# Optimization experiments

Measured on AMD Instinct MI355X. Metric: run time of the kernel, lower is better.

The kernel has to match this reference:

```python
import jax, jax.numpy as jnp
import numpy as np

H, D = 8, 32            # num_heads, per-head out_dim (same for C1/C2/C3/state)
ALPHA = 0.2             # leaky-relu negative slope
N_C, N_S = 10000, 1024  # nodes per C type, state nodes
E_CC, E_CS = 120000, 10000
IN_C, IN_S = 128, 64


def setup_inputs() -> dict:
    key = jax.random.key(0)
    ks = jax.random.split(key, 20)
    xn = lambda k, sh, s=1.0: jax.random.normal(k, sh, dtype=jnp.float32) * s
    inp = {}
    inp["feat_C1"] = xn(ks[0], (N_C, IN_C))
    inp["feat_C2"] = xn(ks[1], (N_C, IN_C))
    inp["feat_C3"] = xn(ks[2], (N_C, IN_C))
    inp["feat_state"] = xn(ks[3], (N_S, IN_S))
    # linear weights (xavier-ish scale) and zero biases
    inp["W_node"] = xn(ks[4], (3, IN_C, H * D), 0.06)
    inp["b_node"] = jnp.zeros((3, H * D), jnp.float32)
    inp["W_cc"] = xn(ks[5], (9, IN_C, H * D), 0.06)
    inp["b_cc"] = jnp.zeros((9, H * D), jnp.float32)
    inp["W_cs"] = xn(ks[6], (3, IN_C, H * D), 0.06)
    inp["b_cs"] = jnp.zeros((3, H * D), jnp.float32)
    inp["W_in"] = xn(ks[7], (IN_S, H * D), 0.08)
    inp["b_in"] = jnp.zeros((H * D,), jnp.float32)
    # attention vectors: [..., 0] = src vec, [..., 1] = dst vec
    inp["attn_cc"] = xn(ks[8], (9, 2, H, D), 0.3)
    inp["attn_cs"] = xn(ks[9], (3, 2, H, D), 0.3)
    # edge lists; relation r = 3*src_type + dst_type for cc
    inp["edges_cc_src"] = jax.random.randint(ks[10], (9, E_CC), 0, N_C, dtype=jnp.int32)
    inp["edges_cc_dst"] = jax.random.randint(ks[11], (9, E_CC), 0, N_C, dtype=jnp.int32)
    inp["edges_cs_src"] = jax.random.randint(ks[12], (3, E_CS), 0, N_C, dtype=jnp.int32)
    inp["edges_cs_dst"] = jax.random.randint(ks[13], (3, E_CS), 0, N_S, dtype=jnp.int32)
    return inp


def _segment_softmax(e, dst, n):
    # e: [E, H]; softmax over edges sharing the same dst node (DGL edge_softmax)
    m = jax.ops.segment_max(e, dst, num_segments=n)
    ex = jnp.exp(e - m[dst])
    s = jax.ops.segment_sum(ex, dst, num_segments=n)
    return ex / s[dst]


def _gat_relation(Wh_src, Wh_dst_self, a_src_vec, a_dst_vec, src, dst, n_dst):
    # Wh_src: [Ns,H,D] projected src feats for this relation
    # Wh_dst_self: [Nd,H,D] dst-type self projection (used for dst attention)
    a_s = jnp.sum(Wh_src * a_src_vec, axis=-1)       # [Ns,H]
    a_d = jnp.sum(Wh_dst_self * a_dst_vec, axis=-1)  # [Nd,H]
    e = jax.nn.leaky_relu(a_s[src] + a_d[dst], ALPHA)   # [E,H]
    a = _segment_softmax(e, dst, n_dst)                 # [E,H]
    msg = Wh_src[src] * a[:, :, None]                   # [E,H,D]
    return jax.ops.segment_sum(msg, dst, num_segments=n_dst)


def _forward(feat_C1, feat_C2, feat_C3, feat_state, W_node, b_node, W_cc, b_cc,
             W_cs, b_cs, W_in, b_in, attn_cc, attn_cs,
             edges_cc_src, edges_cc_dst, edges_cs_src, edges_cs_dst):
    feats_c = [feat_C1, feat_C2, feat_C3]
    n_c = [f.shape[0] for f in feats_c]
    # self projections (used as dst attention features)
    Wh_node = [(feats_c[t] @ W_node[t] + b_node[t]).reshape(-1, H, D) for t in range(3)]
    out_c = [jnp.zeros_like(Wh_node[t]) for t in range(3)]
    # 9 C->C relations: r = 3*s + d
    for r in range(9):
        s, d = divmod(r, 3)
        Wh = (feats_c[s] @ W_cc[r] + b_cc[r]).reshape(-1, H, D)
        ft = _gat_relation(Wh, Wh_node[d], attn_cc[r, 0], attn_cc[r, 1],
                           edges_cc_src[r], edges_cc_dst[r], n_c[d])
        out_c[d] = out_c[d] + ft
    # state: 'in' self projection + 3 C->state relations
    Wh_in = (feat_state @ W_in + b_in).reshape(-1, H, D)
    out_s = Wh_in
    n_s = feat_state.shape[0]
    for t in range(3):
        Wh = (feats_c[t] @ W_cs[t] + b_cs[t]).reshape(-1, H, D)
        ft = _gat_relation(Wh, Wh_in, attn_cs[t, 0], attn_cs[t, 1],
                           edges_cs_src[t], edges_cs_dst[t], n_s)
        out_s = out_s + ft
    relu = jax.nn.relu
    return (relu(out_c[0]), relu(out_c[1]), relu(out_c[2]), relu(out_s))


def reference(feat_C1, feat_C2, feat_C3, feat_state, W_node, b_node, W_cc, b_cc,
              W_cs, b_cs, W_in, b_in, attn_cc, attn_cs,
              edges_cc_src, edges_cc_dst, edges_cs_src, edges_cs_dst):
    return _forward(feat_C1, feat_C2, feat_C3, feat_state, W_node, b_node, W_cc,
                    b_cc, W_cs, b_cs, W_in, b_in, attn_cc, attn_cs,
                    edges_cc_src, edges_cc_dst, edges_cs_src, edges_cs_dst)
```

## Files before the change

### kernel.cpp

```cpp
#include <hip/hip_runtime.h>


#define H_ 8
#define D_ 32
#define HD 256
#define NC 10000
#define NS 1024
#define INC 128
#define INS 64
#define ECC 120000
#define ECS 10000
#define ALPHA 0.2f
#define CAP 64

typedef unsigned short u16;
typedef __attribute__((ext_vector_type(8))) short short8;
typedef __attribute__((ext_vector_type(4))) float f32x4;
typedef __attribute__((ext_vector_type(2))) float f32x2;

static constexpr size_t WHB_CC = 0;
static constexpr size_t WHB_CS = 23040000;
static constexpr size_t WHB_IN = 30720000;
static constexpr size_t FB0  = 15491072;
static constexpr size_t ASCC = FB0;
static constexpr size_t ADCC = FB0 + 720000;
static constexpr size_t ASCS = FB0 + 1440000;
static constexpr size_t ADCS = FB0 + 1680000;
static constexpr size_t BAF  = FB0 + 1704576;
static constexpr size_t FBC  = 34437760;
static constexpr size_t FBS  = 38277760;
static constexpr size_t WTCC = 38343296;
static constexpr size_t WTCS = 38638208;
static constexpr size_t WTIN = 38736512;
static constexpr size_t WAT  = 38752896;
static constexpr size_t IBYTE = 77768704;
static constexpr size_t SBYTE = 78140992;

static constexpr int TOTE  = 9 * ECC + 3 * ECS;
static constexpr int NB_Z0 = 91;
static constexpr int NB_FT = 3814;
static constexpr int NB_WT = 104;
static constexpr int NB_FO = 32;
static constexpr int NB_K2 = 2710;

__device__ __forceinline__ u16 f2b(float f) {
  unsigned u = __float_as_uint(f);
  return (u16)((u + 0x7FFFu + ((u >> 16) & 1u)) >> 16);
}
__device__ __forceinline__ float bl(unsigned u) { return __uint_as_float(u << 16); }
__device__ __forceinline__ float bh(unsigned u) { return __uint_as_float(u & 0xffff0000u); }

__global__ __launch_bounds__(256) void k_prep(
    const float* f1, const float* f2, const float* f3, const float* fs,
    const float* Wcc, const float* Wcs, const float* Win, const float* Wnode,
    const float* bcc, const float* bnode, const float* bcs, const float* bin,
    const float* accv, const float* acsv,
    u16* wsu, float* wsf, int* cnts) {
  __shared__ float Ls[64 * 65];
  int b = blockIdx.x, t = threadIdx.x;
  if (b < NB_Z0) {
    int i = b * 256 + t;
    if (i < 23268) ((int4*)cnts)[i] = make_int4(0, 0, 0, 0);
    return;
  }
  b -= NB_Z0;
  if (b < NB_FT) {
    const float* src; u16* dst; int idx, n4;
    if (b < 3750) {
      int ty = b / 1250;
      src = (ty == 0) ? f1 : (ty == 1) ? f2 : f3;
      dst = wsu + FBC + (size_t)ty * 1280000;
      idx = (b - ty * 1250) * 256 + t; n4 = 320000;
    } else {
      src = fs; dst = wsu + FBS; idx = (b - 3750) * 256 + t; n4 = 16384;
    }
    if (idx < n4) {
      float4 v = ((const float4*)src)[idx];
      uint2 o;
      o.x = (unsigned)f2b(v.x) | ((unsigned)f2b(v.y) << 16);
      o.y = (unsigned)f2b(v.z) | ((unsigned)f2b(v.w) << 16);
      *(uint2*)(dst + (size_t)idx * 4) = o;
    }
    return;
  }
  b -= NB_FT;
  if (b < NB_WT) {
    int mat = b >> 3, sub = b & 7;
    int K = (mat == 12) ? INS : INC;
    if (mat == 12 && sub >= 4) return;
    int k0 = (sub >> 2) * 64, n0 = (sub & 3) * 64;
    const float* src; u16* dst;
    if (mat < 9)        { src = Wcc + (size_t)mat * INC * HD;        dst = wsu + WTCC + (size_t)mat * 32768; }
    else if (mat < 12)  { src = Wcs + (size_t)(mat - 9) * INC * HD;  dst = wsu + WTCS + (size_t)(mat - 9) * 32768; }
    else                { src = Win;                                 dst = wsu + WTIN; }
    #pragma unroll
    for (int it = 0; it < 4; it++) {
      int idx = t + it * 256;
      int r = idx >> 4, c4 = idx & 15;
      float4 v = *(const float4*)&src[(size_t)(k0 + r) * HD + n0 + c4 * 4];
      Ls[r * 65 + c4 * 4 + 0] = v.x; Ls[r * 65 + c4 * 4 + 1] = v.y;
      Ls[r * 65 + c4 * 4 + 2] = v.z; Ls[r * 65 + c4 * 4 + 3] = v.w;
    }
    __syncthreads();
    int n = t >> 2, k8 = (t & 3) * 16;
    unsigned o[8];
    #pragma unroll
    for (int j = 0; j < 8; j++) {
      u16 lo = f2b(Ls[(k8 + 2 * j) * 65 + n]);
      u16 hi = f2b(Ls[(k8 + 2 * j + 1) * 65 + n]);
      o[j] = (unsigned)lo | ((unsigned)hi << 16);
    }
    uint4* dp = (uint4*)&dst[(size_t)(n0 + n) * K + k0 + k8];
    dp[0] = make_uint4(o[0], o[1], o[2], o[3]);
    dp[1] = make_uint4(o[4], o[5], o[6], o[7]);
    return;
  }
  b -= NB_WT;
  int tile = b >> 3, sub = b & 7;
  int K = (tile == 3) ? INS : INC;
  int c0 = sub * 8;
  for (int idx = t; idx < 8 * K; idx += 256) {
    int col = c0 + idx / K, k = idx % K;
    int m = col >> 3, h = col & 7;
    const float* W = nullptr; const float* av = nullptr;
    if (tile < 3) {
      if (m < 3)      { int r = 3*tile + m; W = Wcc + (size_t)r*INC*HD;   av = accv + (size_t)r*512 + h*32; }
      else if (m < 6) { int r = 3*(m-3) + tile; W = Wnode + (size_t)tile*INC*HD; av = accv + (size_t)r*512 + 256 + h*32; }
      else if (m == 6){ W = Wcs + (size_t)tile*INC*HD; av = acsv + (size_t)tile*512 + h*32; }
    } else if (m < 3) { W = Win; av = acsv + (size_t)m*512 + 256 + h*32; }
    float s = 0.f;
    if (W) {
      const float* wp = W + (size_t)k * HD + h * 32;
      #pragma unroll 8
      for (int d = 0; d < 32; d++) s += wp[d] * av[d];
    }
    wsu[WAT + (size_t)tile * 8192 + (size_t)col * K + k] = f2b(s);
  }
  if (sub == 0 && t < 64) {
    int col = t, m = col >> 3, h = col & 7;
    const float* bb = nullptr; const float* av = nullptr;
    if (tile < 3) {
      if (m < 3)      { int r = 3*tile + m; bb = bcc + (size_t)r*HD;  av = accv + (size_t)r*512 + h*32; }
      else if (m < 6) { int r = 3*(m-3) + tile; bb = bnode + (size_t)tile*HD; av = accv + (size_t)r*512 + 256 + h*32; }
      else if (m == 6){ bb = bcs + (size_t)tile*HD; av = acsv + (size_t)tile*512 + h*32; }
    } else if (m < 3) { bb = bin; av = acsv + (size_t)m*512 + 256 + h*32; }
    float s = 0.f;
    if (bb) for (int d = 0; d < 32; d++) s += bb[h*32 + d] * av[d];
    wsf[BAF + tile * 64 + col] = s;
  }
}

__global__ __launch_bounds__(256, 2) void k_fuse(
    u16* wsu, float* wsf, const float* bcc, const float* bcs, const float* bin,
    const int* eccs, const int* eccd, const int* ecss, const int* ecsd,
    int* cnts, u16* slt) {
  __shared__ __align__(16) char smem[69632];
  int gb = blockIdx.x, t = threadIdx.x;
  if ((gb % 5) == 4) {
    int k = gb / 5;
    int i0 = (k * 256 + t) * 8;
    if (i0 >= TOTE) return;
    int dd[8], ss[8], p[8];
    int cbase;
    if (i0 < 9 * ECC) {
      int r = i0 / ECC;
      int4 d0 = *(const int4*)&eccd[i0]; int4 d1 = *(const int4*)&eccd[i0 + 4];
      int4 s0 = *(const int4*)&eccs[i0]; int4 s1 = *(const int4*)&eccs[i0 + 4];
      dd[0]=d0.x; dd[1]=d0.y; dd[2]=d0.z; dd[3]=d0.w;
      dd[4]=d1.x; dd[5]=d1.y; dd[6]=d1.z; dd[7]=d1.w;
      ss[0]=s0.x; ss[1]=s0.y; ss[2]=s0.z; ss[3]=s0.w;
      ss[4]=s1.x; ss[5]=s1.y; ss[6]=s1.z; ss[7]=s1.w;
      cbase = r * NC;
    } else {
      int u0 = i0 - 9 * ECC;
      int r = u0 / ECS;
      int4 d0 = *(const int4*)&ecsd[u0]; int4 d1 = *(const int4*)&ecsd[u0 + 4];
      int4 s0 = *(const int4*)&ecss[u0]; int4 s1 = *(const int4*)&ecss[u0 + 4];
      dd[0]=d0.x; dd[1]=d0.y; dd[2]=d0.z; dd[3]=d0.w;
      dd[4]=d1.x; dd[5]=d1.y; dd[6]=d1.z; dd[7]=d1.w;
      ss[0]=s0.x; ss[1]=s0.y; ss[2]=s0.z; ss[3]=s0.w;
      ss[4]=s1.x; ss[5]=s1.y; ss[6]=s1.z; ss[7]=s1.w;
      cbase = 90000 + r * NS;
    }
    #pragma unroll
    for (int q = 0; q < 8; q++) p[q] = atomicAdd(&cnts[cbase + dd[q]], 1);
    #pragma unroll
    for (int q = 0; q < 8; q++)
      if (p[q] < CAP) slt[((size_t)(cbase + dd[q])) * CAP + p[q]] = (u16)ss[q];
    return;
  }
  int g = 4 * (gb / 5) + (gb % 5);
  if (g >= 2157) return;
  u16* As = (u16*)smem;
  u16* Bs = (u16*)(smem + 34816);
  const u16 *A, *Bt; const float* bias = nullptr; u16* C = nullptr;
  int M, K, r0, n0 = 0, ty = 0;
  bool isScore = false;
  if (g < 1896) {
    int z = g / 158, rem = g - z * 158;
    int by = rem / 79, bx = rem - by * 79;
    r0 = bx * 128; n0 = by * 128; M = NC; K = 128;
    if (z < 9) { A = wsu + FBC + (size_t)(z/3)*1280000; Bt = wsu + WTCC + (size_t)z*32768; bias = bcc + (size_t)z*HD; C = wsu + WHB_CC + (size_t)z*NC*HD; }
    else { int q = z - 9; A = wsu + FBC + (size_t)q*1280000; Bt = wsu + WTCS + (size_t)q*32768; bias = bcs + (size_t)q*HD; C = wsu + WHB_CS + (size_t)q*NC*HD; }
  } else if (g < 1912) {
    int loc = g - 1896; int by = loc / 8, bx = loc - by * 8;
    r0 = bx * 128; n0 = by * 128; M = NS; K = 64;
    A = wsu + FBS; Bt = wsu + WTIN; bias = bin; C = wsu + WHB_IN;
  } else if (g < 2149) {
    isScore = true; ty = (g - 1912) / 79; int bx = (g - 1912) % 79;
    r0 = bx * 128; M = NC; K = 128;
    A = wsu + FBC + (size_t)ty * 1280000; Bt = wsu + WAT + (size_t)ty * 8192;
  } else {
    isScore = true; ty = 3; int bx = g - 2149;
    r0 = bx * 128; M = NS; K = 64;
    A = wsu + FBS; Bt = wsu + WAT + (size_t)3 * 8192;
  }
  int SA = K + 8;
  int NB = isScore ? 64 : 128;
  {
    int ksh = (K == 128) ? 4 : 3;
    int kmask = (1 << ksh) - 1;
    int sc8 = SA >> 3;
    const uint4* ga = (const uint4*)(A + (size_t)r0 * K);
    const uint4* gb2 = (const uint4*)(Bt + (size_t)n0 * K);
    uint4* la = (uint4*)As; uint4* lb = (uint4*)Bs;
    int tota = (128 * K) >> 3, totb = (NB * K) >> 3;
    for (int i = t; i < tota; i += 256) la[(i >> ksh) * sc8 + (i & kmask)] = ga[i];
    for (int i = t; i < totb; i += 256) lb[(i >> ksh) * sc8 + (i & kmask)] = gb2[i];
  }
  __syncthreads();
  int lane = t & 63, w = t >> 6, l16 = lane & 15, quad = lane >> 4;
  int arow0 = w * 32 + l16;
  if (!isScore) {
    f32x4 acc[2][8];
    #pragma unroll
    for (int i = 0; i < 2; i++)
      #pragma unroll
      for (int j = 0; j < 8; j++) acc[i][j] = (f32x4){0.f, 0.f, 0.f, 0.f};
    for (int ks = 0; ks < K; ks += 32) {
      int ko = ks + quad * 8;
      short8 a0 = *(const short8*)&As[(size_t)arow0 * SA + ko];
      short8 a1 = *(const short8*)&As[(size_t)(arow0 + 16) * SA + ko];
      #pragma unroll
      for (int j = 0; j < 8; j++) {
        short8 bfr = *(const short8*)&Bs[(size_t)(j * 16 + l16) * SA + ko];
        acc[0][j] = __builtin_amdgcn_mfma_f32_16x16x32_bf16(a0, bfr, acc[0][j], 0, 0, 0);
        acc[1][j] = __builtin_amdgcn_mfma_f32_16x16x32_bf16(a1, bfr, acc[1][j], 0, 0, 0);
      }
    }
    __syncthreads();
    float* Cl = (float*)smem;
    #pragma unroll
    for (int i = 0; i < 2; i++) {
      int rl0 = w * 32 + i * 16 + quad * 4;
      #pragma unroll
      for (int j = 0; j < 8; j++) {
        int cl = j * 16 + l16;
        float bv = bias[n0 + cl];
        #pragma unroll
        for (int rg = 0; rg < 4; rg++)
          Cl[(rl0 + rg) * 132 + cl] = acc[i][j][rg] + bv;
      }
    }
    __syncthreads();
    for (int task = t; task < 2048; task += 256) {
      int row = task >> 4, seg = task & 15;
      int gr = r0 + row;
      if (gr >= M) continue;
      const float* cp = Cl + row * 132 + seg * 8;
      float4 v0 = *(const float4*)cp;
      float4 v1 = *(const float4*)(cp + 4);
      uint4 o;
      o.x = (unsigned)f2b(v0.x) | ((unsigned)f2b(v0.y) << 16);
      o.y = (unsigned)f2b(v0.z) | ((unsigned)f2b(v0.w) << 16);
      o.z = (unsigned)f2b(v1.x) | ((unsigned)f2b(v1.y) << 16);
      o.w = (unsigned)f2b(v1.z) | ((unsigned)f2b(v1.w) << 16);
      *(uint4*)&C[(size_t)gr * HD + n0 + seg * 8] = o;
    }
  } else {
    f32x4 acc[2][4];
    #pragma unroll
    for (int i = 0; i < 2; i++)
      #pragma unroll
      for (int j = 0; j < 4; j++) acc[i][j] = (f32x4){0.f, 0.f, 0.f, 0.f};
    for (int ks = 0; ks < K; ks += 32) {
      int ko = ks + quad * 8;
      short8 a0 = *(const short8*)&As[(size_t)arow0 * SA + ko];
      short8 a1 = *(const short8*)&As[(size_t)(arow0 + 16) * SA + ko];
      #pragma unroll
      for (int j = 0; j < 4; j++) {
        short8 bfr = *(const short8*)&Bs[(size_t)(j * 16 + l16) * SA + ko];
        acc[0][j] = __builtin_amdgcn_mfma_f32_16x16x32_bf16(a0, bfr, acc[0][j], 0, 0, 0);
        acc[1][j] = __builtin_amdgcn_mfma_f32_16x16x32_bf16(a1, bfr, acc[1][j], 0, 0, 0);
      }
    }
    float* sp[4]; float bav[4];
    #pragma unroll
    for (int j = 0; j < 4; j++) {
      int col = j * 16 + l16;
      int m = col >> 3, h = col & 7;
      float* p = nullptr;
      if (ty < 3) {
        if (m < 3)       p = wsf + ASCC + (size_t)(3*ty + m) * NC * H_;
        else if (m < 6)  p = wsf + ADCC + (size_t)(3*(m-3) + ty) * NC * H_;
        else if (m == 6) p = wsf + ASCS + (size_t)ty * NC * H_;
      } else if (m < 3)  p = wsf + ADCS + (size_t)m * NS * H_;
      sp[j] = p ? (p + h) : nullptr;
      bav[j] = wsf[BAF + ty * 64 + col];
    }
    #pragma unroll
    for (int i = 0; i < 2; i++) {
      int rl0 = w * 32 + i * 16 + quad * 4;
      #pragma unroll
      for (int j = 0; j < 4; j++) {
        if (!sp[j]) continue;
        #pragma unroll
        for (int rg = 0; rg < 4; rg++) {
          int gr = r0 + rl0 + rg;
          if (gr < M) sp[j][(size_t)gr * 8] = (acc[i][j][rg] + bav[j]) * 1.44269504089f;
        }
      }
    }
  }
}

__device__ __forceinline__ void loadg8(uint2* buf, int srcv, int cl, int g,
                                       const char* wb, int lb) {
  #pragma unroll
  for (int ee = 0; ee < 8; ee++) {
    int sre = __builtin_amdgcn_readlane(srcv, min(g + ee, cl));
    buf[ee] = *(const uint2*)(wb + ((size_t)(unsigned)sre << 9) + lb);
  }
}
__device__ __forceinline__ void consume8(const uint2* buf, const float* wp,
                                         f32x2& sA, f32x2& sB) {
  #pragma unroll
  for (int ee = 0; ee < 8; ee++) {
    float wv = wp[ee * 8];
    f32x2 q0, q1;
    q0.x = bl(buf[ee].x); q0.y = bh(buf[ee].x);
    q1.x = bl(buf[ee].y); q1.y = bh(buf[ee].y);
    sA += q0 * wv;
    sB += q1 * wv;
  }
}

__global__ __launch_bounds__(256) void k_agg(const u16* wsu, const float* wsf,
                                             const int* cnts, const u16* slt,
                                             float* out) {
  __shared__ float Wsm[4 * 1536];
  int t = threadIdx.x, lane = t & 63, w = t >> 6;
  int node = blockIdx.x * 4 + w;
  int l3 = lane >> 3, h7 = lane & 7;
  int lb = lane * 8;
  float* Wv = Wsm + w * 1536;
  bool isC = node < 3 * NC;
  int dtype = 0, n;
  if (isC) { dtype = node / NC; n = node - dtype * NC; } else { n = node - 3 * NC; }

  int cidx[3]; const float* ASp[3]; const float* adnp[3]; const char* wb[3];
  #pragma unroll
  for (int j = 0; j < 3; j++) {
    if (isC) {
      int r = j * 3 + dtype;
      cidx[j] = r * NC + n;
      ASp[j]  = wsf + ASCC + (size_t)r * NC * H_;
      adnp[j] = wsf + ADCC + (size_t)r * NC * H_ + (size_t)n * H_ + h7;
      wb[j]   = (const char*)(wsu + WHB_CC + (size_t)r * NC * HD);
    } else {
      cidx[j] = 90000 + j * NS + n;
      ASp[j]  = wsf + ASCS + (size_t)j * NC * H_;
      adnp[j] = wsf + ADCS + (size_t)j * NS * H_ + (size_t)n * H_ + h7;
      wb[j]   = (const char*)(wsu + WHB_CS + (size_t)j * NC * HD);
    }
  }
  int cnt[3], clm[3], srcv[3]; float adn[3];
  #pragma unroll
  for (int j = 0; j < 3; j++) cnt[j] = min(cnts[cidx[j]], CAP);
  #pragma unroll
  for (int j = 0; j < 3; j++) {
    clm[j] = max(cnt[j] - 1, 0);
    srcv[j] = (int)slt[(size_t)cidx[j] * CAP + min(lane, clm[j])];
  }
  #pragma unroll
  for (int j = 0; j < 3; j++) adn[j] = *adnp[j];

  uint2 cur[8], nxt[8];
  loadg8(cur, srcv[0], clm[0], 0, wb[0], lb);

  float invp[3];
  #pragma unroll
  for (int j = 0; j < 3; j++) {
    float zac = 0.f;
    int c = cnt[j];
    for (int g = 0; g < c; g += 8) {
      int e = g + l3;
      int sid = __shfl(srcv[j], min(e, clm[j]));
      float sc = ASp[j][(size_t)sid * H_ + h7] + adn[j];
      sc = fmaxf(sc, ALPHA * sc);
      float wv = (e < c) ? __builtin_amdgcn_exp2f(sc) : 0.f;
      zac += wv;
      Wv[j * 512 + g * 8 + lane] = wv;
    }
    zac += __shfl_xor(zac, 8);
    zac += __shfl_xor(zac, 16);
    zac += __shfl_xor(zac, 32);
    float inv = 1.f / zac;
    invp[j] = (c > 0) ? __shfl(inv, l3) : 0.f;
  }

  f32x2 tA = {0.f, 0.f}, tB = {0.f, 0.f};
#define RELBODY(J, JN, LAST)                                                 \
  {                                                                          \
    int c = cnt[J];                                                          \
    if (c > 0) {                                                             \
      f32x2 sA = {0.f, 0.f}, sB = {0.f, 0.f};                                \
      for (int g = 0; g < c; g += 8) {                                       \
        if (g + 8 < c) loadg8(nxt, srcv[J], clm[J], g + 8, wb[J], lb);       \
        else if (!(LAST)) loadg8(nxt, srcv[JN], clm[JN], 0, wb[JN], lb);     \
        consume8(cur, Wv + (J) * 512 + g * 8 + l3, sA, sB);                  \
        _Pragma("unroll")                                                    \
        for (int ee = 0; ee < 8; ee++) cur[ee] = nxt[ee];                    \
      }                                                                      \
      tA += sA * invp[J];                                                    \
      tB += sB * invp[J];                                                    \
    } else if (!(LAST)) {                                                    \
      loadg8(cur, srcv[JN], clm[JN], 0, wb[JN], lb);                         \
    }                                                                        \
  }
  RELBODY(0, 1, false)
  RELBODY(1, 2, false)
  RELBODY(2, 2, true)
#undef RELBODY

  if (!isC) {
    uint2 m = *(const uint2*)((const char*)(wsu + WHB_IN) + (size_t)n * 512 + lb);
    tA.x += bl(m.x); tA.y += bh(m.x);
    tB.x += bl(m.y); tB.y += bh(m.y);
  }
  float4 v = make_float4(fmaxf(tA.x, 0.f), fmaxf(tA.y, 0.f),
                         fmaxf(tB.x, 0.f), fmaxf(tB.y, 0.f));
  *(float4*)(out + (size_t)node * HD + lane * 4) = v;
}

extern "C" void kernel_launch(void* const* d_in, const int* in_sizes, int n_in,
                              void* d_out, int out_size, void* d_ws, size_t ws_size,
                              hipStream_t stream) {
  (void)in_sizes; (void)n_in; (void)out_size; (void)ws_size;
  const float* f1    = (const float*)d_in[0];
  const float* f2    = (const float*)d_in[1];
  const float* f3    = (const float*)d_in[2];
  const float* fs    = (const float*)d_in[3];
  const float* Wnode = (const float*)d_in[4];
  const float* bnode = (const float*)d_in[5];
  const float* Wcc   = (const float*)d_in[6];
  const float* bcc   = (const float*)d_in[7];
  const float* Wcs   = (const float*)d_in[8];
  const float* bcs   = (const float*)d_in[9];
  const float* Win   = (const float*)d_in[10];
  const float* bin   = (const float*)d_in[11];
  const float* accv  = (const float*)d_in[12];
  const float* acsv  = (const float*)d_in[13];
  const int* eccs    = (const int*)d_in[14];
  const int* eccd    = (const int*)d_in[15];
  const int* ecss    = (const int*)d_in[16];
  const int* ecsd    = (const int*)d_in[17];
  float* wsf = (float*)d_ws;
  u16*   wsu = (u16*)d_ws;
  int*   cnts = (int*)((char*)d_ws + IBYTE);
  u16*   slt  = (u16*)((char*)d_ws + SBYTE);
  float* out = (float*)d_out;

  k_prep<<<dim3(NB_Z0 + NB_FT + NB_WT + NB_FO), 256, 0, stream>>>(
      f1, f2, f3, fs, Wcc, Wcs, Win, Wnode, bcc, bnode, bcs, bin, accv, acsv,
      wsu, wsf, cnts);
  k_fuse<<<dim3(NB_K2), 256, 0, stream>>>(
      wsu, wsf, bcc, bcs, bin, eccs, eccd, ecss, ecsd, cnts, slt);
  k_agg<<<dim3((3 * NC + NS) / 4), 256, 0, stream>>>(wsu, wsf, cnts, slt, out);
}
```

Measured before the change: 265.5 us.

## Fuse softmax score pass into aggregation loop using shuffles instead of LDS

```diff
diff --git a/kernel.cpp b/kernel.cpp
--- a/kernel.cpp
+++ b/kernel.cpp
@@ -324,19 +324,19 @@
   }
 }
 
-__device__ __forceinline__ void loadg8(uint2* buf, int srcv, int cl, int g,
-                                       const char* wb, int lb) {
+__device__ __forceinline__ void loadg8(uint2* buf, const char* wb, int srcv,
+                                       int cl, int g, int lb) {
   #pragma unroll
   for (int ee = 0; ee < 8; ee++) {
     int sre = __builtin_amdgcn_readlane(srcv, min(g + ee, cl));
     buf[ee] = *(const uint2*)(wb + ((size_t)(unsigned)sre << 9) + lb);
   }
 }
-__device__ __forceinline__ void consume8(const uint2* buf, const float* wp,
+__device__ __forceinline__ void consume8(const uint2* buf, float wold, int l3,
                                          f32x2& sA, f32x2& sB) {
   #pragma unroll
   for (int ee = 0; ee < 8; ee++) {
-    float wv = wp[ee * 8];
+    float wv = __shfl(wold, ee * 8 + l3);
     f32x2 q0, q1;
     q0.x = bl(buf[ee].x); q0.y = bh(buf[ee].x);
     q1.x = bl(buf[ee].y); q1.y = bh(buf[ee].y);
@@ -344,16 +344,22 @@
     sB += q1 * wv;
   }
 }
+__device__ __forceinline__ float score8(const float* ASp, float adn, int srcv,
+                                        int cl, int c, int g, int l3, int h7) {
+  int e = g + l3;
+  int sid = __shfl(srcv, min(e, cl));
+  float sc = ASp[(size_t)sid * H_ + h7] + adn;
+  sc = fmaxf(sc, ALPHA * sc);
+  return (e < c) ? __builtin_amdgcn_exp2f(sc) : 0.f;
+}
 
 __global__ __launch_bounds__(256) void k_agg(const u16* wsu, const float* wsf,
                                              const int* cnts, const u16* slt,
                                              float* out) {
-  __shared__ float Wsm[4 * 1536];
   int t = threadIdx.x, lane = t & 63, w = t >> 6;
   int node = blockIdx.x * 4 + w;
   int l3 = lane >> 3, h7 = lane & 7;
   int lb = lane * 8;
-  float* Wv = Wsm + w * 1536;
   bool isC = node < 3 * NC;
   int dtype = 0, n;
   if (isC) { dtype = node / NC; n = node - dtype * NC; } else { n = node - 3 * NC; }
@@ -374,59 +380,54 @@
       wb[j]   = (const char*)(wsu + WHB_CS + (size_t)j * NC * HD);
     }
   }
-  int cnt[3], clm[3], srcv[3]; float adn[3];
+  int srcv[3]; float adn[3]; int cnt[3], clm[3];
+  #pragma unroll
+  for (int j = 0; j < 3; j++) srcv[j] = (int)slt[(size_t)cidx[j] * CAP + lane];
+  #pragma unroll
+  for (int j = 0; j < 3; j++) adn[j] = *adnp[j];
   #pragma unroll
   for (int j = 0; j < 3; j++) cnt[j] = min(cnts[cidx[j]], CAP);
   #pragma unroll
-  for (int j = 0; j < 3; j++) {
-    clm[j] = max(cnt[j] - 1, 0);
-    srcv[j] = (int)slt[(size_t)cidx[j] * CAP + min(lane, clm[j])];
-  }
-  #pragma unroll
-  for (int j = 0; j < 3; j++) adn[j] = *adnp[j];
+  for (int j = 0; j < 3; j++) clm[j] = max(cnt[j] - 1, 0);
 
   uint2 cur[8], nxt[8];
-  loadg8(cur, srcv[0], clm[0], 0, wb[0], lb);
-
-  float invp[3];
-  #pragma unroll
-  for (int j = 0; j < 3; j++) {
-    float zac = 0.f;
-    int c = cnt[j];
-    for (int g = 0; g < c; g += 8) {
-      int e = g + l3;
-      int sid = __shfl(srcv[j], min(e, clm[j]));
-      float sc = ASp[j][(size_t)sid * H_ + h7] + adn[j];
-      sc = fmaxf(sc, ALPHA * sc);
-      float wv = (e < c) ? __builtin_amdgcn_exp2f(sc) : 0.f;
-      zac += wv;
-      Wv[j * 512 + g * 8 + lane] = wv;
-    }
-    zac += __shfl_xor(zac, 8);
-    zac += __shfl_xor(zac, 16);
-    zac += __shfl_xor(zac, 32);
-    float inv = 1.f / zac;
-    invp[j] = (c > 0) ? __shfl(inv, l3) : 0.f;
-  }
+  loadg8(cur, wb[0], srcv[0], clm[0], 0, lb);
+  float wcur = score8(ASp[0], adn[0], srcv[0], clm[0], cnt[0], 0, l3, h7);
 
   f32x2 tA = {0.f, 0.f}, tB = {0.f, 0.f};
-#define RELBODY(J, JN, LAST)                                                 \
-  {                                                                          \
-    int c = cnt[J];                                                          \
-    if (c > 0) {                                                             \
-      f32x2 sA = {0.f, 0.f}, sB = {0.f, 0.f};                                \
-      for (int g = 0; g < c; g += 8) {                                       \
-        if (g + 8 < c) loadg8(nxt, srcv[J], clm[J], g + 8, wb[J], lb);       \
-        else if (!(LAST)) loadg8(nxt, srcv[JN], clm[JN], 0, wb[JN], lb);     \
-        consume8(cur, Wv + (J) * 512 + g * 8 + l3, sA, sB);                  \
-        _Pragma("unroll")                                                    \
-        for (int ee = 0; ee < 8; ee++) cur[ee] = nxt[ee];                    \
-      }                                                                      \
-      tA += sA * invp[J];                                                    \
-      tB += sB * invp[J];                                                    \
-    } else if (!(LAST)) {                                                    \
-      loadg8(cur, srcv[JN], clm[JN], 0, wb[JN], lb);                         \
-    }                                                                        \
+#define RELBODY(J, JN, LAST)                                                  \
+  {                                                                           \
+    int c = cnt[J];                                                           \
+    if (c > 0) {                                                              \
+      f32x2 sA = {0.f, 0.f}, sB = {0.f, 0.f};                                 \
+      float zac = 0.f;                                                        \
+      for (int g = 0; g < c; g += 8) {                                        \
+        if (g + 8 < c)                                                        \
+          loadg8(nxt, wb[J], srcv[J], clm[J], g + 8, lb);                     \
+        else if (!(LAST))                                                     \
+          loadg8(nxt, wb[JN], srcv[JN], clm[JN], 0, lb);                      \
+        float wold = wcur;                                                    \
+        zac += wold;                                                          \
+        if (g + 8 < c)                                                        \
+          wcur = score8(ASp[J], adn[J], srcv[J], clm[J], c, g + 8, l3, h7);   \
+        consume8(cur, wold, l3, sA, sB);                                      \
+        _Pragma("unroll")                                                     \
+        for (int ee = 0; ee < 8; ee++) cur[ee] = nxt[ee];                     \
+      }                                                                       \
+      zac += __shfl_xor(zac, 8);                                              \
+      zac += __shfl_xor(zac, 16);                                             \
+      zac += __shfl_xor(zac, 32);                                             \
+      float inv = 1.f / zac;                                                  \
+      float invp = __shfl(inv, l3);                                           \
+      tA += sA * invp;                                                        \
+      tB += sB * invp;                                                        \
+      if (!(LAST) && cnt[JN] > 0)                                             \
+        wcur = score8(ASp[JN], adn[JN], srcv[JN], clm[JN], cnt[JN], 0, l3, h7); \
+    } else if (!(LAST)) {                                                     \
+      loadg8(cur, wb[JN], srcv[JN], clm[JN], 0, lb);                          \
+      if (cnt[JN] > 0)                                                        \
+        wcur = score8(ASp[JN], adn[JN], srcv[JN], clm[JN], cnt[JN], 0, l3, h7); \
+    }                                                                         \
   }
   RELBODY(0, 1, false)
   RELBODY(1, 2, false)
```

After: 261.6 us. Within noise of the previous version (-1.4%).
